# Optimization experiments

Hardware: AMD Instinct MI355X
Metric: run time of the kernel (lower is better)

## Reference

```python
import jax, jax.numpy as jnp
import numpy as np

N_NODES = 100000
HIDDEN = 128
N_EDGES = 1000000


def setup_inputs() -> dict:
    key = jax.random.key(0)
    k1, k2, k3 = jax.random.split(key, 3)
    z = jax.random.normal(k1, (N_NODES, HIDDEN), dtype=jnp.float32)
    edge_index = jax.random.randint(k2, (2, N_EDGES), 0, N_NODES, dtype=jnp.int64)
    # xavier_uniform for square matrix: bound = sqrt(6/(fan_in+fan_out))
    bound = float(np.sqrt(6.0 / (HIDDEN + HIDDEN)))
    weights = jax.random.uniform(k3, (HIDDEN, HIDDEN), dtype=jnp.float32,
                                 minval=-bound, maxval=bound)
    return {"z": z, "edge_index": edge_index, "weights": weights}


def reference(z, edge_index, weights):
    # symm=True: symmetrize the bilinear form
    W = weights + weights.T                      # [d, d]
    z_src = z[edge_index[0]]                     # [E, d] gather
    z_dst = z[edge_index[1]]                     # [E, d] gather
    # torch: (W @ z_dst.T).T == z_dst @ W.T
    value = jnp.einsum('ed,dk,ek->e', z_src, W, z_dst)  # row-wise bilinear score
    return jax.nn.sigmoid(value)
```

## Files before the change

### kernel.cpp

```cpp
#include <hip/hip_runtime.h>

#define HIDDEN 128
#define LDSW 136

typedef _Float16 f16;
typedef f16 f16x2 __attribute__((ext_vector_type(2)));
typedef f16 f16x8 __attribute__((ext_vector_type(8)));
typedef float f32x16 __attribute__((ext_vector_type(16)));

static __device__ __forceinline__ float fdot2(f16x2 a, f16x2 b, float c) {
    return __builtin_amdgcn_fdot2(a, b, c, false);
}

__global__ __launch_bounds__(256) void prep_w(const float* __restrict__ w,
                                              f16* __restrict__ wsh_t) {
    int idx = blockIdx.x * 256 + threadIdx.x;
    int j = idx >> 7, k = idx & 127;
    wsh_t[idx] = (f16)(w[k * HIDDEN + j] + w[j * HIDDEN + k]);
}

__global__ __launch_bounds__(256) void gemm_mfma(const float* __restrict__ z,
                                                 const f16* __restrict__ wsh_t,
                                                 f16* __restrict__ zh,
                                                 f16* __restrict__ uh, int nrows) {
    __shared__ f16 wlt[HIDDEN * LDSW];
    int tid = threadIdx.x;
    {
        const f16x8* g = (const f16x8*)wsh_t;
        #pragma unroll
        for (int it = 0; it < 8; ++it) {
            int idx = it * 256 + tid;
            int j = idx >> 4, kc = idx & 15;
            *(f16x8*)&wlt[j * LDSW + kc * 8] = g[idx];
        }
    }
    __syncthreads();

    int wave = tid >> 6, lane = tid & 63;
    int row0 = blockIdx.x * 128 + wave * 32;
    if (row0 > nrows - 32) row0 = nrows - 32;

    int m = lane & 31, half = lane >> 5;
    const float* zr = z  + (size_t)(row0 + m) * HIDDEN + half * 8;
    f16*        zhr = zh + (size_t)(row0 + m) * HIDDEN + half * 8;
    const f16* wbase = &wlt[m * LDSW + half * 8];

    f32x16 acc0 = {0.f}, acc1 = {0.f}, acc2 = {0.f}, acc3 = {0.f};
    #pragma unroll
    for (int r = 0; r < 16; ++r) { acc0[r] = 0.f; acc1[r] = 0.f; acc2[r] = 0.f; acc3[r] = 0.f; }

    #pragma unroll
    for (int ks = 0; ks < 8; ++ks) {
        float4 a0 = *(const float4*)(zr + 16 * ks);
        float4 a1 = *(const float4*)(zr + 16 * ks + 4);
        f16x8 af = {(f16)a0.x, (f16)a0.y, (f16)a0.z, (f16)a0.w,
                    (f16)a1.x, (f16)a1.y, (f16)a1.z, (f16)a1.w};
        *(f16x8*)(zhr + 16 * ks) = af;
        f16x8 b0 = *(const f16x8*)(wbase + 16 * ks);
        f16x8 b1 = *(const f16x8*)(wbase + 32 * LDSW + 16 * ks);
        f16x8 b2 = *(const f16x8*)(wbase + 64 * LDSW + 16 * ks);
        f16x8 b3 = *(const f16x8*)(wbase + 96 * LDSW + 16 * ks);
        acc0 = __builtin_amdgcn_mfma_f32_32x32x16_f16(af, b0, acc0, 0, 0, 0);
        acc1 = __builtin_amdgcn_mfma_f32_32x32x16_f16(af, b1, acc1, 0, 0, 0);
        acc2 = __builtin_amdgcn_mfma_f32_32x32x16_f16(af, b2, acc2, 0, 0, 0);
        acc3 = __builtin_amdgcn_mfma_f32_32x32x16_f16(af, b3, acc3, 0, 0, 0);
    }

    f16* ur = uh + (size_t)row0 * HIDDEN;
    #pragma unroll
    for (int r = 0; r < 16; ++r) {
        int row = (r & 3) + 8 * (r >> 2) + 4 * half;
        f16* p = ur + (size_t)row * HIDDEN + m;
        p[0]  = (f16)acc0[r];
        p[32] = (f16)acc1[r];
        p[64] = (f16)acc2[r];
        p[96] = (f16)acc3[r];
    }
}

__global__ __launch_bounds__(256) void edge_score4(const f16* __restrict__ uh,
                                                   const f16* __restrict__ zh,
                                                   const int* __restrict__ eidx,
                                                   float* __restrict__ out, int E) {
    int tid = threadIdx.x;
    int g = tid >> 2, t = tid & 3;
    int e = blockIdx.x * 64 + g;
    if (e >= E) return;
    int src = eidx[e];
    int dst = eidx[E + e];
    const float4* a4 = (const float4*)(uh + (size_t)src * HIDDEN);
    const float4* b4 = (const float4*)(zh + (size_t)dst * HIDDEN);
    float4 av[4], bv[4];
    #pragma unroll
    for (int i = 0; i < 4; ++i) { av[i] = a4[t + 4 * i]; bv[i] = b4[t + 4 * i]; }
    float s = 0.f;
    #pragma unroll
    for (int i = 0; i < 4; ++i) {
        const f16x2* ap = (const f16x2*)&av[i];
        const f16x2* bp = (const f16x2*)&bv[i];
        #pragma unroll
        for (int j = 0; j < 4; ++j) s = fdot2(ap[j], bp[j], s);
    }
    s += __shfl_xor(s, 1);
    s += __shfl_xor(s, 2);
    if (t == 0) out[e] = 1.0f / (1.0f + __expf(-s));
}

extern "C" void kernel_launch(void* const* d_in, const int* in_sizes, int n_in,
                              void* d_out, int out_size, void* d_ws, size_t ws_size,
                              hipStream_t stream) {
    const float* z    = (const float*)d_in[0];
    const int*   eidx = (const int*)d_in[1];
    const float* w    = (const float*)d_in[2];
    float* out = (float*)d_out;

    int nrows = in_sizes[0] / HIDDEN;
    int E = out_size;

    f16* wsh_t = (f16*)d_ws;
    f16* zh    = wsh_t + HIDDEN * HIDDEN;
    f16* uh    = zh + (size_t)nrows * HIDDEN;

    prep_w<<<(HIDDEN * HIDDEN) / 256, 256, 0, stream>>>(w, wsh_t);
    gemm_mfma<<<(nrows + 127) / 128, 256, 0, stream>>>(z, wsh_t, zh, uh, nrows);
    edge_score4<<<(E + 63) / 64, 256, 0, stream>>>(uh, zh, eidx, out, E);
}
```

Measured before the change: 175.2 us.

## Stage z tile in LDS for MFMA and use 16 threads per edge

The GEMM now loads each 128-row tile of z with coalesced float4 reads, converts it to fp16, writes zh, and stages it in LDS in MFMA A-fragment order. W fragments are read straight from global memory or cache instead of being copied into LDS, and launch bounds request 3 blocks per CU. The edge kernel gives each edge 16 threads that each load one 16-byte chunk, which spreads the gathers across more lanes and makes per-lane accesses contiguous, at the cost of more threads and a deeper shuffle reduction. This adds a second LDS pass in the GEMM, and W loads now depend on cache hits.

Measured after the change: 177.3 us. No clear change (+1.2%).

```diff
diff --git a/kernel.cpp b/kernel.cpp
--- a/kernel.cpp
+++ b/kernel.cpp
@@ -1,7 +1,7 @@
 #include <hip/hip_runtime.h>
 
 #define HIDDEN 128
-#define LDSW 136
+#define SLOT_H 264
 
 typedef _Float16 f16;
 typedef f16 f16x2 __attribute__((ext_vector_type(2)));
@@ -15,58 +15,60 @@
 __global__ __launch_bounds__(256) void prep_w(const float* __restrict__ w,
                                               f16* __restrict__ wsh_t) {
     int idx = blockIdx.x * 256 + threadIdx.x;
-    int j = idx >> 7, k = idx & 127;
-    wsh_t[idx] = (f16)(w[k * HIDDEN + j] + w[j * HIDDEN + k]);
+    int n = idx >> 7, k = idx & 127;
+    wsh_t[idx] = (f16)(w[k * HIDDEN + n] + w[n * HIDDEN + k]);
 }
 
-__global__ __launch_bounds__(256) void gemm_mfma(const float* __restrict__ z,
-                                                 const f16* __restrict__ wsh_t,
-                                                 f16* __restrict__ zh,
-                                                 f16* __restrict__ uh, int nrows) {
-    __shared__ f16 wlt[HIDDEN * LDSW];
+__global__ __launch_bounds__(256, 3) void gemm_mfma2(const float* __restrict__ z,
+                                                     const f16* __restrict__ wsh_t,
+                                                     f16* __restrict__ zh,
+                                                     f16* __restrict__ uh, int nrows) {
+    __shared__ f16 afrag[64 * SLOT_H];
     int tid = threadIdx.x;
+    int row0 = blockIdx.x * 128;
+    if (row0 > nrows - 128) row0 = nrows - 128;
+
     {
-        const f16x8* g = (const f16x8*)wsh_t;
+        const float4* zg = (const float4*)(z + (size_t)row0 * HIDDEN);
+        f16x8* zhg = (f16x8*)(zh + (size_t)row0 * HIDDEN);
         #pragma unroll
         for (int it = 0; it < 8; ++it) {
-            int idx = it * 256 + tid;
-            int j = idx >> 4, kc = idx & 15;
-            *(f16x8*)&wlt[j * LDSW + kc * 8] = g[idx];
+            int g = it * 256 + tid;
+            float4 v0 = zg[2 * g];
+            float4 v1 = zg[2 * g + 1];
+            f16x8 h = {(f16)v0.x, (f16)v0.y, (f16)v0.z, (f16)v0.w,
+                       (f16)v1.x, (f16)v1.y, (f16)v1.z, (f16)v1.w};
+            zhg[g] = h;
+            int row = g >> 4, ch = g & 15;
+            int slot = (row >> 5) * 16 + ch;
+            *(f16x8*)&afrag[slot * SLOT_H + (row & 31) * 8] = h;
         }
     }
     __syncthreads();
 
     int wave = tid >> 6, lane = tid & 63;
-    int row0 = blockIdx.x * 128 + wave * 32;
-    if (row0 > nrows - 32) row0 = nrows - 32;
+    int m = lane & 31, half = lane >> 5;
 
-    int m = lane & 31, half = lane >> 5;
-    const float* zr = z  + (size_t)(row0 + m) * HIDDEN + half * 8;
-    f16*        zhr = zh + (size_t)(row0 + m) * HIDDEN + half * 8;
-    const f16* wbase = &wlt[m * LDSW + half * 8];
+    const f16* wb = wsh_t + (size_t)m * HIDDEN + half * 8;
 
-    f32x16 acc0 = {0.f}, acc1 = {0.f}, acc2 = {0.f}, acc3 = {0.f};
+    f32x16 acc0, acc1, acc2, acc3;
     #pragma unroll
     for (int r = 0; r < 16; ++r) { acc0[r] = 0.f; acc1[r] = 0.f; acc2[r] = 0.f; acc3[r] = 0.f; }
 
     #pragma unroll
     for (int ks = 0; ks < 8; ++ks) {
-        float4 a0 = *(const float4*)(zr + 16 * ks);
-        float4 a1 = *(const float4*)(zr + 16 * ks + 4);
-        f16x8 af = {(f16)a0.x, (f16)a0.y, (f16)a0.z, (f16)a0.w,
-                    (f16)a1.x, (f16)a1.y, (f16)a1.z, (f16)a1.w};
-        *(f16x8*)(zhr + 16 * ks) = af;
-        f16x8 b0 = *(const f16x8*)(wbase + 16 * ks);
-        f16x8 b1 = *(const f16x8*)(wbase + 32 * LDSW + 16 * ks);
-        f16x8 b2 = *(const f16x8*)(wbase + 64 * LDSW + 16 * ks);
-        f16x8 b3 = *(const f16x8*)(wbase + 96 * LDSW + 16 * ks);
-        acc0 = __builtin_amdgcn_mfma_f32_32x32x16_f16(af, b0, acc0, 0, 0, 0);
-        acc1 = __builtin_amdgcn_mfma_f32_32x32x16_f16(af, b1, acc1, 0, 0, 0);
-        acc2 = __builtin_amdgcn_mfma_f32_32x32x16_f16(af, b2, acc2, 0, 0, 0);
-        acc3 = __builtin_amdgcn_mfma_f32_32x32x16_f16(af, b3, acc3, 0, 0, 0);
+        f16x8 a = *(const f16x8*)&afrag[(wave * 16 + ks * 2 + half) * SLOT_H + m * 8];
+        f16x8 b0 = *(const f16x8*)&wb[ 0 * HIDDEN + 16 * ks];
+        f16x8 b1 = *(const f16x8*)&wb[32 * HIDDEN + 16 * ks];
+        f16x8 b2 = *(const f16x8*)&wb[64 * HIDDEN + 16 * ks];
+        f16x8 b3 = *(const f16x8*)&wb[96 * HIDDEN + 16 * ks];
+        acc0 = __builtin_amdgcn_mfma_f32_32x32x16_f16(a, b0, acc0, 0, 0, 0);
+        acc1 = __builtin_amdgcn_mfma_f32_32x32x16_f16(a, b1, acc1, 0, 0, 0);
+        acc2 = __builtin_amdgcn_mfma_f32_32x32x16_f16(a, b2, acc2, 0, 0, 0);
+        acc3 = __builtin_amdgcn_mfma_f32_32x32x16_f16(a, b3, acc3, 0, 0, 0);
     }
 
-    f16* ur = uh + (size_t)row0 * HIDDEN;
+    f16* ur = uh + (size_t)(row0 + wave * 32) * HIDDEN;
     #pragma unroll
     for (int r = 0; r < 16; ++r) {
         int row = (r & 3) + 8 * (r >> 2) + 4 * half;
@@ -78,31 +80,26 @@
     }
 }
 
-__global__ __launch_bounds__(256) void edge_score4(const f16* __restrict__ uh,
-                                                   const f16* __restrict__ zh,
-                                                   const int* __restrict__ eidx,
-                                                   float* __restrict__ out, int E) {
+__global__ __launch_bounds__(256) void edge_score16(const f16* __restrict__ uh,
+                                                    const f16* __restrict__ zh,
+                                                    const int* __restrict__ eidx,
+                                                    float* __restrict__ out, int E) {
     int tid = threadIdx.x;
-    int g = tid >> 2, t = tid & 3;
-    int e = blockIdx.x * 64 + g;
+    int g = tid >> 4, t = tid & 15;
+    int e = blockIdx.x * 16 + g;
     if (e >= E) return;
     int src = eidx[e];
     int dst = eidx[E + e];
     const float4* a4 = (const float4*)(uh + (size_t)src * HIDDEN);
     const float4* b4 = (const float4*)(zh + (size_t)dst * HIDDEN);
-    float4 av[4], bv[4];
-    #pragma unroll
-    for (int i = 0; i < 4; ++i) { av[i] = a4[t + 4 * i]; bv[i] = b4[t + 4 * i]; }
+    float4 av = a4[t], bv = b4[t];
+    const f16x2* ap = (const f16x2*)&av;
+    const f16x2* bp = (const f16x2*)&bv;
     float s = 0.f;
     #pragma unroll
-    for (int i = 0; i < 4; ++i) {
-        const f16x2* ap = (const f16x2*)&av[i];
-        const f16x2* bp = (const f16x2*)&bv[i];
-        #pragma unroll
-        for (int j = 0; j < 4; ++j) s = fdot2(ap[j], bp[j], s);
-    }
-    s += __shfl_xor(s, 1);
-    s += __shfl_xor(s, 2);
+    for (int i = 0; i < 4; ++i) s = fdot2(ap[i], bp[i], s);
+    #pragma unroll
+    for (int off = 8; off > 0; off >>= 1) s += __shfl_down(s, off, 16);
     if (t == 0) out[e] = 1.0f / (1.0f + __expf(-s));
 }
 
@@ -122,6 +119,6 @@
     f16* uh    = zh + (size_t)nrows * HIDDEN;
 
     prep_w<<<(HIDDEN * HIDDEN) / 256, 256, 0, stream>>>(w, wsh_t);
-    gemm_mfma<<<(nrows + 127) / 128, 256, 0, stream>>>(z, wsh_t, zh, uh, nrows);
-    edge_score4<<<(E + 63) / 64, 256, 0, stream>>>(uh, zh, eidx, out, E);
+    gemm_mfma2<<<(nrows + 127) / 128, 256, 0, stream>>>(z, wsh_t, zh, uh, nrows);
+    edge_score16<<<(E + 15) / 16, 256, 0, stream>>>(uh, zh, eidx, out, E);
 }
```
